# Kernel tuning notes

Measured on AMD Instinct MI355X. Metric: run time of the kernel, lower is better.

Reference implementation:

```python
import jax, jax.numpy as jnp
import numpy as np

N, E, H = 50000, 800000, 64  # nodes, edges, hidden
EPS = 1e-5
SLOPE = 0.2  # LeakyReLU negative slope


def setup_inputs() -> dict:
    key = jax.random.key(0)
    ks = jax.random.split(key, 8)
    return {
        "x": jax.random.normal(ks[0], (N, H), dtype=jnp.float32),
        "edge_weight": jax.random.uniform(ks[1], (E,), dtype=jnp.float32),
        "edge_index": jax.random.randint(ks[2], (2, E), 0, N, dtype=jnp.int64),
        # Linear weights, torch convention [out_features, in_features], bias=False
        "w1": jax.random.normal(ks[3], (H, 2 * H), dtype=jnp.float32) * 0.05,
        "w2": jax.random.normal(ks[4], (H, H), dtype=jnp.float32) * 0.05,
        "w3": jax.random.normal(ks[5], (H, H), dtype=jnp.float32) * 0.05,
        # LayerNorm affine params
        "g1": jnp.ones((2 * H,), jnp.float32), "b1": jnp.zeros((2 * H,), jnp.float32),
        "g2": jnp.ones((H,), jnp.float32), "b2": jnp.zeros((H,), jnp.float32),
        "g3": jnp.ones((H,), jnp.float32), "b3": jnp.zeros((H,), jnp.float32),
    }


def _ln_act_lin(h, g, b, w):
    # LayerNorm -> LeakyReLU(0.2) -> Linear(bias=False), as in MLP(norm='layer')
    mu = jnp.mean(h, axis=-1, keepdims=True)
    var = jnp.mean((h - mu) ** 2, axis=-1, keepdims=True)
    h = (h - mu) * jax.lax.rsqrt(var + EPS) * g + b
    h = jnp.where(h > 0, h, SLOPE * h)
    return h @ w.T


def reference(x, edge_weight, edge_index, w1, w2, w3, g1, b1, g2, b2, g3, b3):
    src, tgt = edge_index[0], edge_index[1]  # x_j = source, x_i = target
    x_j = x[src]                              # [E, H] gather
    x_i = x[tgt]                              # [E, H] gather
    m = jnp.concatenate([x_i, edge_weight[:, None] * (x_j - x_i)], axis=-1)  # [E, 2H]
    m = _ln_act_lin(m, g1, b1, w1)
    m = _ln_act_lin(m, g2, b2, w2)
    m = _ln_act_lin(m, g3, b3, w3)            # [E, H]
    agg = jax.ops.segment_max(m, tgt, num_segments=N)  # EdgeConv aggr='max'
    agg = jnp.where(jnp.isfinite(agg), agg, 0.0)       # isolated nodes -> 0
    return agg + x                             # residual (ResBlock)
```

## Files before the change

kernel.cpp:

```cpp
#include <hip/hip_runtime.h>

#define NN 50000
#define NE 800000
#define NT (NE / 32)

#define CNT_OFF   0u
#define BASE_OFF  204800u
#define PART_OFF  409600u
#define SLOT_OFF  417792u
#define SRCW_OFF  3670016u
#define M_OFF     (1u << 24)
#define WS_NEEDED ((size_t)(1u << 24) + (size_t)NE * 64u * 2u)
#define PB 196

typedef __bf16 bf16x8 __attribute__((ext_vector_type(8)));
typedef float f32x16 __attribute__((ext_vector_type(16)));

union U4 { unsigned u[4]; __bf16 h[8]; bf16x8 v; };

__device__ __forceinline__ unsigned pkpair(float a, float b) {
  union { unsigned u; __bf16 h[2]; } r;
  r.h[0] = (__bf16)a; r.h[1] = (__bf16)b;
  return r.u;
}
__device__ __forceinline__ float bflo(unsigned u) { return __uint_as_float(u << 16); }
__device__ __forceinline__ float bfhi(unsigned u) { return __uint_as_float(u & 0xFFFF0000u); }

extern "C" __global__ void __launch_bounds__(256)
scatter_kernel(const int* __restrict__ ei, unsigned* __restrict__ cnt,
               unsigned* __restrict__ slot) {
  const int e = blockIdx.x * 256 + threadIdx.x;
  if (e < NE) {
    int t = ei[NE + e];
    t = min(max(t, 0), NN - 1);
    slot[e] = atomicAdd(cnt + t, 1u);
  }
}

extern "C" __global__ void __launch_bounds__(256)
scan_a_kernel(const unsigned* __restrict__ cnt, unsigned* __restrict__ partial) {
  __shared__ unsigned wsum[4];
  const int t = threadIdx.x, wv = t >> 6, ln = t & 63;
  const int i = blockIdx.x * 256 + t;
  unsigned v = (i < NN) ? cnt[i] : 0u;
  #pragma unroll
  for (int d = 1; d < 64; d <<= 1) v += (unsigned)__shfl_up((int)v, d) * (ln >= d ? 1u : 0u);
  if (ln == 63) wsum[wv] = v;
  __syncthreads();
  if (t == 0) partial[blockIdx.x] = wsum[0] + wsum[1] + wsum[2] + wsum[3];
}

extern "C" __global__ void __launch_bounds__(256)
scan_b_kernel(unsigned* __restrict__ partial, unsigned* __restrict__ base) {
  __shared__ unsigned wsum[4];
  const int t = threadIdx.x, wv = t >> 6, ln = t & 63;
  const unsigned v = (t < PB) ? partial[t] : 0u;
  unsigned s = v;
  #pragma unroll
  for (int d = 1; d < 64; d <<= 1) s += (unsigned)__shfl_up((int)s, d) * (ln >= d ? 1u : 0u);
  if (ln == 63) wsum[wv] = s;
  __syncthreads();
  unsigned woff = 0;
  #pragma unroll
  for (int k = 0; k < 4; ++k) woff += (k < wv) ? wsum[k] : 0u;
  if (t < PB) partial[t] = woff + s - v;
  if (t == 255) base[NN] = woff + s;
}

extern "C" __global__ void __launch_bounds__(256)
scan_c_kernel(const unsigned* __restrict__ cnt, const unsigned* __restrict__ partial,
              unsigned* __restrict__ base) {
  __shared__ unsigned wsum[4];
  const int t = threadIdx.x, wv = t >> 6, ln = t & 63;
  const int i = blockIdx.x * 256 + t;
  const unsigned v = (i < NN) ? cnt[i] : 0u;
  unsigned s = v;
  #pragma unroll
  for (int d = 1; d < 64; d <<= 1) s += (unsigned)__shfl_up((int)s, d) * (ln >= d ? 1u : 0u);
  if (ln == 63) wsum[wv] = s;
  __syncthreads();
  unsigned woff = 0;
  #pragma unroll
  for (int k = 0; k < 4; ++k) woff += (k < wv) ? wsum[k] : 0u;
  if (i < NN) base[i] = partial[blockIdx.x] + woff + s - v;
}

extern "C" __global__ void __launch_bounds__(256)
reorder_kernel(const int* __restrict__ ei, const float* __restrict__ ew,
               const unsigned* __restrict__ base, const unsigned* __restrict__ slot,
               uint4* __restrict__ srcw) {
  const int e = blockIdx.x * 256 + threadIdx.x;
  if (e < NE) {
    const int s = min(max(ei[e], 0), NN - 1);
    const int t = min(max(ei[NE + e], 0), NN - 1);
    const unsigned pos = base[t] + slot[e];
    uint4 rec;
    rec.x = (unsigned)s; rec.y = (unsigned)t;
    rec.z = __float_as_uint(ew[e]); rec.w = 0u;
    srcw[pos] = rec;
  }
}

extern "C" __global__ void __launch_bounds__(256, 3)
edge_mlp_kernel(const float* __restrict__ x, const float* __restrict__ w1,
                const float* __restrict__ w2, const float* __restrict__ w3,
                const float* __restrict__ g1, const float* __restrict__ b1,
                const float* __restrict__ g2, const float* __restrict__ b2,
                const float* __restrict__ g3, const float* __restrict__ b3,
                const uint4* __restrict__ srcw,
                unsigned short* __restrict__ pmax) {
  __shared__ unsigned lds_w[8192];
  __shared__ float lds_p[512];
  const int tid = threadIdx.x;

  #pragma unroll 1
  for (int s = tid; s < 1024; s += 256) {
    const int F = s >> 6, L = s & 63;
    const int t = F >> 1, mt = F & 1;
    const int gg = L >> 5, o = (L & 31) + 32 * mt;
    const float* p = w1 + o * 128 + 16 * t + 8 * gg;
    unsigned* d = &lds_w[(unsigned)(F * 64 + L) * 4u];
    d[0] = pkpair(p[0], p[1]); d[1] = pkpair(p[2], p[3]);
    d[2] = pkpair(p[4], p[5]); d[3] = pkpair(p[6], p[7]);
  }
  #pragma unroll 1
  for (int s = tid; s < 1024; s += 256) {
    const int which = s >> 9, r = s & 511;
    const int F = r >> 6, L = r & 63;
    const int t = F >> 1, mt = F & 1;
    const int gg = L >> 5, o = (L & 31) + 32 * mt;
    const float* W = which ? w3 : w2;
    const float* p = W + o * 64 + 16 * t + 4 * gg;
    unsigned* d = &lds_w[(unsigned)((16 + which * 8 + F) * 64 + L) * 4u];
    d[0] = pkpair(p[0], p[1]); d[1] = pkpair(p[2], p[3]);
    d[2] = pkpair(p[8], p[9]); d[3] = pkpair(p[10], p[11]);
  }
  #pragma unroll 1
  for (int s = tid; s < 512; s += 256) {
    float v;
    if (s < 128)      v = g1[s];
    else if (s < 256) v = b1[s - 128];
    else if (s < 320) v = g2[s - 256];
    else if (s < 384) v = b2[s - 320];
    else if (s < 448) v = g3[s - 384];
    else              v = b3[s - 448];
    lds_p[s] = v;
  }
  __syncthreads();

  const int lane = tid & 63;
  const int el = lane & 31;
  const int g = lane >> 5;
  const bf16x8* wfrag = (const bf16x8*)lds_w;

  const int wid = blockIdx.x * 4 + (tid >> 6);
  const int nw = gridDim.x * 4;

  int tile = wid;
  int pvs = 0, pvt = 0; float pw = 0.f;
  if (tile < NT) {
    const uint4 rec = srcw[tile * 32 + el];
    pvs = (int)rec.x; pvt = (int)rec.y; pw = __uint_as_float(rec.z);
  }

  while (tile < NT) {
    asm volatile("" ::: "memory");

    const int p = tile * 32 + el;
    const int vsrc = pvs, vtgt = pvt;
    const float wgt = pw;

    const float* xi = x + (size_t)vtgt * 64 + 8 * g;
    const float* xj = x + (size_t)vsrc * 64 + 8 * g;

    unsigned mp[32];
    float sum = 0.f, ssq = 0.f;
    #pragma unroll
    for (int t = 0; t < 4; ++t) {
      float4 a = *(const float4*)(xi + 16 * t);
      float4 b = *(const float4*)(xi + 16 * t + 4);
      float4 c = *(const float4*)(xj + 16 * t);
      float4 d4 = *(const float4*)(xj + 16 * t + 4);
      float lo[8] = {a.x, a.y, a.z, a.w, b.x, b.y, b.z, b.w};
      float up[8] = {wgt * (c.x - a.x), wgt * (c.y - a.y), wgt * (c.z - a.z), wgt * (c.w - a.w),
                     wgt * (d4.x - b.x), wgt * (d4.y - b.y), wgt * (d4.z - b.z), wgt * (d4.w - b.w)};
      #pragma unroll
      for (int pp = 0; pp < 4; ++pp) {
        mp[4 * t + pp] = pkpair(lo[2 * pp], lo[2 * pp + 1]);
        mp[16 + 4 * t + pp] = pkpair(up[2 * pp], up[2 * pp + 1]);
      }
      #pragma unroll
      for (int j = 0; j < 8; ++j) {
        sum += lo[j] + up[j];
        ssq += lo[j] * lo[j] + up[j] * up[j];
      }
    }

    const int ntile = tile + nw;
    if (ntile < NT) {
      const uint4 rec = srcw[ntile * 32 + el];
      pvs = (int)rec.x; pvt = (int)rec.y; pw = __uint_as_float(rec.z);
    }

    sum += __shfl_xor(sum, 32);
    ssq += __shfl_xor(ssq, 32);
    const float mean1 = sum * (1.f / 128.f);
    const float rstd1 = rsqrtf(ssq * (1.f / 128.f) - mean1 * mean1 + 1e-5f);
    const float c01 = -mean1 * rstd1;

    U4 B1[8];
    #pragma unroll
    for (int t = 0; t < 8; ++t) {
      const int kb = ((t < 4) ? 16 * t : 64 + 16 * (t - 4)) + 8 * g;
      float4 ga = *(const float4*)(lds_p + kb);
      float4 gb = *(const float4*)(lds_p + kb + 4);
      float4 ba = *(const float4*)(lds_p + 128 + kb);
      float4 bb = *(const float4*)(lds_p + 128 + kb + 4);
      float gv[8] = {ga.x, ga.y, ga.z, ga.w, gb.x, gb.y, gb.z, gb.w};
      float bv[8] = {ba.x, ba.y, ba.z, ba.w, bb.x, bb.y, bb.z, bb.w};
      #pragma unroll
      for (int pp = 0; pp < 4; ++pp) {
        const unsigned u = mp[4 * t + pp];
        float v0 = fmaf(bflo(u), rstd1, c01);
        float v1 = fmaf(bfhi(u), rstd1, c01);
        v0 = fmaf(v0, gv[2 * pp], bv[2 * pp]);
        v1 = fmaf(v1, gv[2 * pp + 1], bv[2 * pp + 1]);
        v0 = fmaxf(v0, 0.2f * v0);
        v1 = fmaxf(v1, 0.2f * v1);
        B1[t].h[2 * pp] = (__bf16)v0;
        B1[t].h[2 * pp + 1] = (__bf16)v1;
      }
    }

    f32x16 A0, A1;
    #pragma unroll
    for (int i = 0; i < 16; ++i) { A0[i] = 0.f; A1[i] = 0.f; }
    #pragma unroll
    for (int t = 0; t < 8; ++t) {
      A0 = __builtin_amdgcn_mfma_f32_32x32x16_bf16(wfrag[(2 * t + 0) * 64 + lane], B1[t].v, A0, 0, 0, 0);
      A1 = __builtin_amdgcn_mfma_f32_32x32x16_bf16(wfrag[(2 * t + 1) * 64 + lane], B1[t].v, A1, 0, 0, 0);
    }

    float s2 = 0.f, q2 = 0.f;
    #pragma unroll
    for (int i = 0; i < 16; ++i) {
      s2 += A0[i] + A1[i];
      q2 += A0[i] * A0[i] + A1[i] * A1[i];
    }
    s2 += __shfl_xor(s2, 32); q2 += __shfl_xor(q2, 32);
    const float mean2 = s2 * (1.f / 64.f);
    const float rstd2 = rsqrtf(q2 * (1.f / 64.f) - mean2 * mean2 + 1e-5f);
    const float c02 = -mean2 * rstd2;

    U4 B2[4];
    #pragma unroll
    for (int t2 = 0; t2 < 4; ++t2) {
      const int kb = 16 * t2 + 4 * g;
      float4 gA = *(const float4*)(lds_p + 256 + kb);
      float4 gB = *(const float4*)(lds_p + 256 + kb + 8);
      float4 bA = *(const float4*)(lds_p + 320 + kb);
      float4 bB = *(const float4*)(lds_p + 320 + kb + 8);
      float gv[8] = {gA.x, gA.y, gA.z, gA.w, gB.x, gB.y, gB.z, gB.w};
      float bv[8] = {bA.x, bA.y, bA.z, bA.w, bB.x, bB.y, bB.z, bB.w};
      #pragma unroll
      for (int j = 0; j < 8; ++j) {
        const int reg = 4 * (2 * (t2 & 1) + (j >> 2)) + (j & 3);
        float v = (t2 >> 1) ? A1[reg] : A0[reg];
        v = fmaf(v, rstd2, c02);
        v = fmaf(v, gv[j], bv[j]);
        v = fmaxf(v, 0.2f * v);
        B2[t2].h[j] = (__bf16)v;
      }
    }

    #pragma unroll
    for (int i = 0; i < 16; ++i) { A0[i] = 0.f; A1[i] = 0.f; }
    #pragma unroll
    for (int t2 = 0; t2 < 4; ++t2) {
      A0 = __builtin_amdgcn_mfma_f32_32x32x16_bf16(wfrag[(16 + 2 * t2 + 0) * 64 + lane], B2[t2].v, A0, 0, 0, 0);
      A1 = __builtin_amdgcn_mfma_f32_32x32x16_bf16(wfrag[(16 + 2 * t2 + 1) * 64 + lane], B2[t2].v, A1, 0, 0, 0);
    }

    float s3 = 0.f, q3 = 0.f;
    #pragma unroll
    for (int i = 0; i < 16; ++i) {
      s3 += A0[i] + A1[i];
      q3 += A0[i] * A0[i] + A1[i] * A1[i];
    }
    s3 += __shfl_xor(s3, 32); q3 += __shfl_xor(q3, 32);
    const float mean3 = s3 * (1.f / 64.f);
    const float rstd3 = rsqrtf(q3 * (1.f / 64.f) - mean3 * mean3 + 1e-5f);
    const float c03 = -mean3 * rstd3;

    U4 B3[4];
    #pragma unroll
    for (int t2 = 0; t2 < 4; ++t2) {
      const int kb = 16 * t2 + 4 * g;
      float4 gA = *(const float4*)(lds_p + 384 + kb);
      float4 gB = *(const float4*)(lds_p + 384 + kb + 8);
      float4 bA = *(const float4*)(lds_p + 448 + kb);
      float4 bB = *(const float4*)(lds_p + 448 + kb + 8);
      float gv[8] = {gA.x, gA.y, gA.z, gA.w, gB.x, gB.y, gB.z, gB.w};
      float bv[8] = {bA.x, bA.y, bA.z, bA.w, bB.x, bB.y, bB.z, bB.w};
      #pragma unroll
      for (int j = 0; j < 8; ++j) {
        const int reg = 4 * (2 * (t2 & 1) + (j >> 2)) + (j & 3);
        float v = (t2 >> 1) ? A1[reg] : A0[reg];
        v = fmaf(v, rstd3, c03);
        v = fmaf(v, gv[j], bv[j]);
        v = fmaxf(v, 0.2f * v);
        B3[t2].h[j] = (__bf16)v;
      }
    }

    #pragma unroll
    for (int i = 0; i < 16; ++i) { A0[i] = 0.f; A1[i] = 0.f; }
    #pragma unroll
    for (int t2 = 0; t2 < 4; ++t2) {
      A0 = __builtin_amdgcn_mfma_f32_32x32x16_bf16(wfrag[(24 + 2 * t2 + 0) * 64 + lane], B3[t2].v, A0, 0, 0, 0);
      A1 = __builtin_amdgcn_mfma_f32_32x32x16_bf16(wfrag[(24 + 2 * t2 + 1) * 64 + lane], B3[t2].v, A1, 0, 0, 0);
    }

    unsigned P[16];
    #pragma unroll
    for (int q = 0; q < 4; ++q) {
      P[2 * q + 0] = pkpair(A0[4 * q + 0], A0[4 * q + 1]);
      P[2 * q + 1] = pkpair(A0[4 * q + 2], A0[4 * q + 3]);
      P[8 + 2 * q + 0] = pkpair(A1[4 * q + 0], A1[4 * q + 1]);
      P[8 + 2 * q + 1] = pkpair(A1[4 * q + 2], A1[4 * q + 3]);
    }
    #pragma unroll
    for (int d = 1; d < 32; d <<= 1) {
      const int ot = __shfl_down(vtgt, d, 32);
      const bool mrg = (ot == vtgt);
      #pragma unroll
      for (int i = 0; i < 16; ++i) {
        const unsigned pv = __shfl_down(P[i], d, 32);
        if (mrg) {
          const float a = fmaxf(bflo(P[i]), bflo(pv));
          const float b = fmaxf(bfhi(P[i]), bfhi(pv));
          P[i] = (__float_as_uint(a) >> 16) | (__float_as_uint(b) & 0xFFFF0000u);
        }
      }
    }
    const int pt = __shfl_up(vtgt, 1, 32);
    if (el == 0 || pt != vtgt) {
      unsigned short* row = pmax + (size_t)p * 64;
      #pragma unroll
      for (int q = 0; q < 4; ++q) {
        uint2 lo; lo.x = P[2 * q]; lo.y = P[2 * q + 1];
        uint2 hi; hi.x = P[8 + 2 * q]; hi.y = P[8 + 2 * q + 1];
        *(uint2*)(row + 8 * q + 4 * g) = lo;
        *(uint2*)(row + 32 + 8 * q + 4 * g) = hi;
      }
    }

    tile = ntile;
  }
}

extern "C" __global__ void __launch_bounds__(256)
gather_max_kernel(const float* __restrict__ x, const unsigned short* __restrict__ pmax,
                  const unsigned* __restrict__ base, float* __restrict__ out) {
  const int node = blockIdx.x * 4 + (threadIdx.x >> 6);
  const int lane = threadIdx.x & 63;
  if (node >= NN) return;

  const unsigned b0 = base[node];
  const unsigned b1 = base[node + 1];
  float maxv = -INFINITY;
  if (b1 > b0) {
    maxv = __uint_as_float((unsigned)pmax[(size_t)b0 * 64 + lane] << 16);
    const unsigned k1 = (b1 - 1) >> 5;
    for (unsigned k = (b0 >> 5) + 1; k <= k1; ++k) {
      const float v = __uint_as_float((unsigned)pmax[((size_t)k << 5) * 64 + lane] << 16);
      maxv = fmaxf(maxv, v);
    }
  }
  const size_t o = (size_t)node * 64 + lane;
  out[o] = (maxv >= -3.0e38f ? maxv : 0.f) + x[o];
}

extern "C" void kernel_launch(void* const* d_in, const int* in_sizes, int n_in,
                              void* d_out, int out_size, void* d_ws, size_t ws_size,
                              hipStream_t stream) {
  (void)in_sizes; (void)n_in; (void)out_size; (void)ws_size;
  const float* x  = (const float*)d_in[0];
  const float* ew = (const float*)d_in[1];
  const int*   ei = (const int*)d_in[2];
  const float* w1 = (const float*)d_in[3];
  const float* w2 = (const float*)d_in[4];
  const float* w3 = (const float*)d_in[5];
  const float* g1 = (const float*)d_in[6];
  const float* b1 = (const float*)d_in[7];
  const float* g2 = (const float*)d_in[8];
  const float* b2 = (const float*)d_in[9];
  const float* g3 = (const float*)d_in[10];
  const float* b3 = (const float*)d_in[11];

  unsigned* cnt  = (unsigned*)((char*)d_ws + CNT_OFF);
  unsigned* base = (unsigned*)((char*)d_ws + BASE_OFF);
  unsigned* part = (unsigned*)((char*)d_ws + PART_OFF);
  unsigned* slot = (unsigned*)((char*)d_ws + SLOT_OFF);
  uint4*    srcw = (uint4*)((char*)d_ws + SRCW_OFF);
  unsigned short* pmax = (unsigned short*)((char*)d_ws + M_OFF);

  hipMemsetAsync(cnt, 0, (size_t)NN * sizeof(unsigned), stream);
  scatter_kernel<<<(NE + 255) / 256, 256, 0, stream>>>(ei, cnt, slot);
  scan_a_kernel<<<PB, 256, 0, stream>>>(cnt, part);
  scan_b_kernel<<<1, 256, 0, stream>>>(part, base);
  scan_c_kernel<<<PB, 256, 0, stream>>>(cnt, part, base);
  reorder_kernel<<<(NE + 255) / 256, 256, 0, stream>>>(ei, ew, base, slot, srcw);
  edge_mlp_kernel<<<2048, 256, 0, stream>>>(x, w1, w2, w3,
                                            g1, b1, g2, b2, g3, b3,
                                            srcw, pmax);
  gather_max_kernel<<<(NN + 3) / 4, 256, 0, stream>>>(x, pmax, base, (float*)d_out);
}
```

Before: 278.3 us.

## Fuse scan kernels, pack edge records, use ordered-int bf16 max, widen blocks

Merges the single-block partial scan into the final scan kernel so every block rescans the partial sums itself, which removes one launch. Edge records shrink from 16 to 8 bytes by packing source and target into 16-bit halves, a packing that only holds while N stays below 65536. The segmented max encodes bf16 values as order-preserving unsigned integers so each merge is a packed u16 max with a select instead of unpack, float max and repack, and the gather decodes the result back. The edge MLP kernel moves to 512-thread blocks with a higher occupancy hint, which may increase register pressure.

Result: slower. 340.5 us (+22.3%).

```diff
diff --git a/kernel.cpp b/kernel.cpp
--- a/kernel.cpp
+++ b/kernel.cpp
@@ -15,8 +15,10 @@
 
 typedef __bf16 bf16x8 __attribute__((ext_vector_type(8)));
 typedef float f32x16 __attribute__((ext_vector_type(16)));
+typedef unsigned short u16x2 __attribute__((ext_vector_type(2)));
 
 union U4 { unsigned u[4]; __bf16 h[8]; bf16x8 v; };
+union PKU { unsigned u; u16x2 v; };
 
 __device__ __forceinline__ unsigned pkpair(float a, float b) {
   union { unsigned u; __bf16 h[2]; } r;
@@ -25,6 +27,11 @@
 }
 __device__ __forceinline__ float bflo(unsigned u) { return __uint_as_float(u << 16); }
 __device__ __forceinline__ float bfhi(unsigned u) { return __uint_as_float(u & 0xFFFF0000u); }
+__device__ __forceinline__ unsigned pkmaxu16(unsigned a, unsigned b) {
+  PKU x, y, r; x.u = a; y.u = b;
+  r.v = __builtin_elementwise_max(x.v, y.v);
+  return r.u;
+}
 
 extern "C" __global__ void __launch_bounds__(256)
 scatter_kernel(const int* __restrict__ ei, unsigned* __restrict__ cnt,
@@ -51,11 +58,13 @@
 }
 
 extern "C" __global__ void __launch_bounds__(256)
-scan_b_kernel(unsigned* __restrict__ partial, unsigned* __restrict__ base) {
+scan_c_kernel(const unsigned* __restrict__ cnt, const unsigned* __restrict__ partial,
+              unsigned* __restrict__ base) {
+  __shared__ unsigned pscan[256];
   __shared__ unsigned wsum[4];
   const int t = threadIdx.x, wv = t >> 6, ln = t & 63;
-  const unsigned v = (t < PB) ? partial[t] : 0u;
-  unsigned s = v;
+  const unsigned pv = (t < PB) ? partial[t] : 0u;
+  unsigned s = pv;
   #pragma unroll
   for (int d = 1; d < 64; d <<= 1) s += (unsigned)__shfl_up((int)s, d) * (ln >= d ? 1u : 0u);
   if (ln == 63) wsum[wv] = s;
@@ -63,58 +72,53 @@
   unsigned woff = 0;
   #pragma unroll
   for (int k = 0; k < 4; ++k) woff += (k < wv) ? wsum[k] : 0u;
-  if (t < PB) partial[t] = woff + s - v;
-  if (t == 255) base[NN] = woff + s;
-}
-
-extern "C" __global__ void __launch_bounds__(256)
-scan_c_kernel(const unsigned* __restrict__ cnt, const unsigned* __restrict__ partial,
-              unsigned* __restrict__ base) {
-  __shared__ unsigned wsum[4];
-  const int t = threadIdx.x, wv = t >> 6, ln = t & 63;
+  pscan[t] = woff + s - pv;
+  if (blockIdx.x == 0 && t == 255) base[NN] = woff + s;
+  __syncthreads();
+  const unsigned blockoff = pscan[blockIdx.x];
   const int i = blockIdx.x * 256 + t;
   const unsigned v = (i < NN) ? cnt[i] : 0u;
-  unsigned s = v;
+  unsigned s2 = v;
   #pragma unroll
-  for (int d = 1; d < 64; d <<= 1) s += (unsigned)__shfl_up((int)s, d) * (ln >= d ? 1u : 0u);
-  if (ln == 63) wsum[wv] = s;
+  for (int d = 1; d < 64; d <<= 1) s2 += (unsigned)__shfl_up((int)s2, d) * (ln >= d ? 1u : 0u);
+  if (ln == 63) wsum[wv] = s2;
   __syncthreads();
-  unsigned woff = 0;
+  unsigned woff2 = 0;
   #pragma unroll
-  for (int k = 0; k < 4; ++k) woff += (k < wv) ? wsum[k] : 0u;
-  if (i < NN) base[i] = partial[blockIdx.x] + woff + s - v;
+  for (int k = 0; k < 4; ++k) woff2 += (k < wv) ? wsum[k] : 0u;
+  if (i < NN) base[i] = blockoff + woff2 + s2 - v;
 }
 
 extern "C" __global__ void __launch_bounds__(256)
 reorder_kernel(const int* __restrict__ ei, const float* __restrict__ ew,
                const unsigned* __restrict__ base, const unsigned* __restrict__ slot,
-               uint4* __restrict__ srcw) {
+               uint2* __restrict__ srcw) {
   const int e = blockIdx.x * 256 + threadIdx.x;
   if (e < NE) {
     const int s = min(max(ei[e], 0), NN - 1);
     const int t = min(max(ei[NE + e], 0), NN - 1);
     const unsigned pos = base[t] + slot[e];
-    uint4 rec;
-    rec.x = (unsigned)s; rec.y = (unsigned)t;
-    rec.z = __float_as_uint(ew[e]); rec.w = 0u;
+    uint2 rec;
+    rec.x = (unsigned)s | ((unsigned)t << 16);
+    rec.y = __float_as_uint(ew[e]);
     srcw[pos] = rec;
   }
 }
 
-extern "C" __global__ void __launch_bounds__(256, 3)
+extern "C" __global__ void __launch_bounds__(512, 4)
 edge_mlp_kernel(const float* __restrict__ x, const float* __restrict__ w1,
                 const float* __restrict__ w2, const float* __restrict__ w3,
                 const float* __restrict__ g1, const float* __restrict__ b1,
                 const float* __restrict__ g2, const float* __restrict__ b2,
                 const float* __restrict__ g3, const float* __restrict__ b3,
-                const uint4* __restrict__ srcw,
+                const uint2* __restrict__ srcw,
                 unsigned short* __restrict__ pmax) {
   __shared__ unsigned lds_w[8192];
   __shared__ float lds_p[512];
   const int tid = threadIdx.x;
 
   #pragma unroll 1
-  for (int s = tid; s < 1024; s += 256) {
+  for (int s = tid; s < 1024; s += 512) {
     const int F = s >> 6, L = s & 63;
     const int t = F >> 1, mt = F & 1;
     const int gg = L >> 5, o = (L & 31) + 32 * mt;
@@ -124,7 +128,7 @@
     d[2] = pkpair(p[4], p[5]); d[3] = pkpair(p[6], p[7]);
   }
   #pragma unroll 1
-  for (int s = tid; s < 1024; s += 256) {
+  for (int s = tid; s < 1024; s += 512) {
     const int which = s >> 9, r = s & 511;
     const int F = r >> 6, L = r & 63;
     const int t = F >> 1, mt = F & 1;
@@ -136,7 +140,7 @@
     d[2] = pkpair(p[8], p[9]); d[3] = pkpair(p[10], p[11]);
   }
   #pragma unroll 1
-  for (int s = tid; s < 512; s += 256) {
+  for (int s = tid; s < 512; s += 512) {
     float v;
     if (s < 128)      v = g1[s];
     else if (s < 256) v = b1[s - 128];
@@ -153,14 +157,14 @@
   const int g = lane >> 5;
   const bf16x8* wfrag = (const bf16x8*)lds_w;
 
-  const int wid = blockIdx.x * 4 + (tid >> 6);
-  const int nw = gridDim.x * 4;
+  const int wid = blockIdx.x * 8 + (tid >> 6);
+  const int nw = gridDim.x * 8;
 
   int tile = wid;
   int pvs = 0, pvt = 0; float pw = 0.f;
   if (tile < NT) {
-    const uint4 rec = srcw[tile * 32 + el];
-    pvs = (int)rec.x; pvt = (int)rec.y; pw = __uint_as_float(rec.z);
+    const uint2 rec = srcw[tile * 32 + el];
+    pvs = (int)(rec.x & 0xFFFFu); pvt = (int)(rec.x >> 16); pw = __uint_as_float(rec.y);
   }
 
   while (tile < NT) {
@@ -198,8 +202,8 @@
 
     const int ntile = tile + nw;
     if (ntile < NT) {
-      const uint4 rec = srcw[ntile * 32 + el];
-      pvs = (int)rec.x; pvt = (int)rec.y; pw = __uint_as_float(rec.z);
+      const uint2 rec = srcw[ntile * 32 + el];
+      pvs = (int)(rec.x & 0xFFFFu); pvt = (int)(rec.x >> 16); pw = __uint_as_float(rec.y);
     }
 
     sum += __shfl_xor(sum, 32);
@@ -330,17 +334,20 @@
       P[8 + 2 * q + 1] = pkpair(A1[4 * q + 2], A1[4 * q + 3]);
     }
     #pragma unroll
+    for (int i = 0; i < 16; ++i) {
+      const unsigned u = P[i];
+      const unsigned tt = (u >> 15) & 0x00010001u;
+      P[i] = u ^ ((tt << 15) - tt + 0x80008000u);
+    }
+    #pragma unroll
     for (int d = 1; d < 32; d <<= 1) {
       const int ot = __shfl_down(vtgt, d, 32);
       const bool mrg = (ot == vtgt);
       #pragma unroll
       for (int i = 0; i < 16; ++i) {
         const unsigned pv = __shfl_down(P[i], d, 32);
-        if (mrg) {
-          const float a = fmaxf(bflo(P[i]), bflo(pv));
-          const float b = fmaxf(bfhi(P[i]), bfhi(pv));
-          P[i] = (__float_as_uint(a) >> 16) | (__float_as_uint(b) & 0xFFFF0000u);
-        }
+        const unsigned mx = pkmaxu16(P[i], pv);
+        P[i] = mrg ? mx : P[i];
       }
     }
     const int pt = __shfl_up(vtgt, 1, 32);
@@ -368,17 +375,18 @@
 
   const unsigned b0 = base[node];
   const unsigned b1 = base[node + 1];
-  float maxv = -INFINITY;
+  float maxv = 0.f;
   if (b1 > b0) {
-    maxv = __uint_as_float((unsigned)pmax[(size_t)b0 * 64 + lane] << 16);
+    unsigned kmax = pmax[(size_t)b0 * 64 + lane];
     const unsigned k1 = (b1 - 1) >> 5;
     for (unsigned k = (b0 >> 5) + 1; k <= k1; ++k) {
-      const float v = __uint_as_float((unsigned)pmax[((size_t)k << 5) * 64 + lane] << 16);
-      maxv = fmaxf(maxv, v);
-    }
+      kmax = max(kmax, (unsigned)pmax[((size_t)k << 5) * 64 + lane]);
+    }
+    const unsigned orig = (kmax & 0x8000u) ? (kmax ^ 0x8000u) : (~kmax & 0xFFFFu);
+    maxv = __uint_as_float(orig << 16);
   }
   const size_t o = (size_t)node * 64 + lane;
-  out[o] = (maxv >= -3.0e38f ? maxv : 0.f) + x[o];
+  out[o] = maxv + x[o];
 }
 
 extern "C" void kernel_launch(void* const* d_in, const int* in_sizes, int n_in,
@@ -402,16 +410,15 @@
   unsigned* base = (unsigned*)((char*)d_ws + BASE_OFF);
   unsigned* part = (unsigned*)((char*)d_ws + PART_OFF);
   unsigned* slot = (unsigned*)((char*)d_ws + SLOT_OFF);
-  uint4*    srcw = (uint4*)((char*)d_ws + SRCW_OFF);
+  uint2*    srcw = (uint2*)((char*)d_ws + SRCW_OFF);
   unsigned short* pmax = (unsigned short*)((char*)d_ws + M_OFF);
 
   hipMemsetAsync(cnt, 0, (size_t)NN * sizeof(unsigned), stream);
   scatter_kernel<<<(NE + 255) / 256, 256, 0, stream>>>(ei, cnt, slot);
   scan_a_kernel<<<PB, 256, 0, stream>>>(cnt, part);
-  scan_b_kernel<<<1, 256, 0, stream>>>(part, base);
   scan_c_kernel<<<PB, 256, 0, stream>>>(cnt, part, base);
   reorder_kernel<<<(NE + 255) / 256, 256, 0, stream>>>(ei, ew, base, slot, srcw);
-  edge_mlp_kernel<<<2048, 256, 0, stream>>>(x, w1, w2, w3,
+  edge_mlp_kernel<<<1024, 512, 0, stream>>>(x, w1, w2, w3,
                                             g1, b1, g2, b2, g3, b3,
                                             srcw, pmax);
   gather_max_kernel<<<(NN + 3) / 4, 256, 0, stream>>>(x, pmax, base, (float*)d_out);
```
